# Optimization experiments

Hardware: AMD Instinct MI355X
Metric: run time of the kernel (lower is better)

Reference implementation:

```python
import jax, jax.numpy as jnp
import numpy as np
import math

EMBED = 768
HEADS = 12
DK = EMBED // HEADS
FFN = 3072
NQ = 8
B, S = 4, 2048


def _layernorm(x, g, b, eps=1e-5):
    mu = jnp.mean(x, axis=-1, keepdims=True)
    var = jnp.var(x, axis=-1, keepdims=True)
    return (x - mu) * jax.lax.rsqrt(var + eps) * g + b


def setup_inputs() -> dict:
    key = jax.random.key(0)
    ks = jax.random.split(key, 16)
    std = 0.02
    inp = {
        "x": jax.random.normal(ks[0], (B, S, EMBED), dtype=jnp.float32),
        "mask": jnp.ones((B, S), dtype=jnp.int32),
        # attention projections (torch Linear: W [out, in])
        "wq": jax.random.normal(ks[1], (EMBED, EMBED), jnp.float32) * std,
        "bq": jnp.zeros((EMBED,), jnp.float32),
        "wk": jax.random.normal(ks[2], (EMBED, EMBED), jnp.float32) * std,
        "bk": jnp.zeros((EMBED,), jnp.float32),
        "wv": jax.random.normal(ks[3], (EMBED, EMBED), jnp.float32) * std,
        "bv": jnp.zeros((EMBED,), jnp.float32),
        "wo": jax.random.normal(ks[4], (EMBED, EMBED), jnp.float32) * std,
        "bo": jnp.zeros((EMBED,), jnp.float32),
        # layernorms
        "g1": jnp.ones((EMBED,), jnp.float32),
        "be1": jnp.zeros((EMBED,), jnp.float32),
        "g2": jnp.ones((EMBED,), jnp.float32),
        "be2": jnp.zeros((EMBED,), jnp.float32),
        # quantum FFN: trainable RY angles + two linears
        "theta": jax.random.normal(ks[5], (NQ,), jnp.float32) * 0.1,
        "w1": jax.random.normal(ks[6], (FFN, NQ), jnp.float32) * std,
        "b1": jnp.zeros((FFN,), jnp.float32),
        "w2": jax.random.normal(ks[7], (EMBED, FFN), jnp.float32) * std,
        "b2": jnp.zeros((EMBED,), jnp.float32),
    }
    return inp


def _block(x, mask, wq, bq, wk, bk, wv, bv, wo, bo, g1, be1, g2, be2,
           theta, w1, b1, w2, b2):
    b, s, _ = x.shape
    # --- multi-head attention (dropout = identity at eval) ---
    q = (x @ wq.T + bq).reshape(b, s, HEADS, DK)
    k = (x @ wk.T + bk).reshape(b, s, HEADS, DK)
    v = (x @ wv.T + bv).reshape(b, s, HEADS, DK)
    scores = jnp.einsum("bqhd,bkhd->bhqk", q, k) / math.sqrt(DK)
    scores = jnp.where(mask[:, None, None, :] == 0, -1e9, scores)
    attn = jax.nn.softmax(scores, axis=-1)
    ctx = jnp.einsum("bhqk,bkhd->bqhd", attn, v).reshape(b, s, EMBED)
    attn_out = ctx @ wo.T + bo
    x = _layernorm(x + attn_out, g1, be1)
    # --- quantum FFN: RY(x_i) then RY(theta_i) on |0>, <Z> = cos(x_i+theta_i)
    # (product state, no entanglement -> exact closed form, fully batched)
    meas = jnp.cos(x[..., :NQ] + theta)            # [b, s, NQ]
    h = jax.nn.relu(meas @ w1.T + b1)              # [b, s, FFN]
    ffn_out = h @ w2.T + b2                        # [b, s, EMBED]
    return _layernorm(x + ffn_out, g2, be2)


def reference(x, mask, wq, bq, wk, bk, wv, bv, wo, bo, g1, be1, g2, be2,
              theta, w1, b1, w2, b2):
    return _block(x, mask, wq, bq, wk, bk, wv, bv, wo, bo,
                  g1, be1, g2, be2, theta, w1, b1, w2, b2)
```

## Files before the change

### kernel.cpp

```cpp
#include <hip/hip_runtime.h>
#include <hip/hip_bf16.h>


typedef __bf16 bf16_t;
typedef bf16_t bf16x4 __attribute__((ext_vector_type(4)));
typedef bf16_t bf16x8 __attribute__((ext_vector_type(8)));
typedef float floatx4 __attribute__((ext_vector_type(4)));

#define LOG2E 1.44269504088896f

__device__ __forceinline__ void gload16(const bf16_t* g, bf16_t* l) {
    __builtin_amdgcn_global_load_lds(
        (const __attribute__((address_space(1))) unsigned int*)g,
        (__attribute__((address_space(3))) unsigned int*)l,
        16, 0, 0);
}

__global__ __launch_bounds__(256)
void prep(const float* __restrict__ x,
          const float* __restrict__ wq, const float* __restrict__ wk,
          const float* __restrict__ wv, const float* __restrict__ wo,
          const float* __restrict__ w2, const float* __restrict__ w1,
          const float* __restrict__ bq, const float* __restrict__ bk,
          const float* __restrict__ bv, const int* __restrict__ mask,
          bf16_t* __restrict__ xb, bf16_t* __restrict__ wqkv,
          bf16_t* __restrict__ wob, bf16_t* __restrict__ w2b,
          bf16_t* __restrict__ w1b, float* __restrict__ bqkv,
          float* __restrict__ mbf)
{
    const int seg = blockIdx.y;
    const int idx = blockIdx.x * 256 + threadIdx.x;
    if (seg == 0) {
        if (idx >= 1572864) return;
        const float4 f = ((const float4*)x)[idx];
        bf16x4 o = {(bf16_t)f.x, (bf16_t)f.y, (bf16_t)f.z, (bf16_t)f.w};
        ((bf16x4*)xb)[idx] = o;
    } else if (seg == 1) {
        if (idx >= 442368) return;
        const int e = idx * 4;
        float4 f = (e < 589824) ? ((const float4*)wq)[idx]
                 : (e < 1179648) ? ((const float4*)wk)[idx - 147456]
                                 : ((const float4*)wv)[idx - 294912];
        if (e < 589824) { f.x *= 0.125f; f.y *= 0.125f; f.z *= 0.125f; f.w *= 0.125f; }
        bf16x4 o = {(bf16_t)f.x, (bf16_t)f.y, (bf16_t)f.z, (bf16_t)f.w};
        ((bf16x4*)wqkv)[idx] = o;
    } else if (seg == 2) {
        if (idx >= 147456) return;
        const float4 f = ((const float4*)wo)[idx];
        bf16x4 o = {(bf16_t)f.x, (bf16_t)f.y, (bf16_t)f.z, (bf16_t)f.w};
        ((bf16x4*)wob)[idx] = o;
    } else if (seg == 3) {
        if (idx >= 589824) return;
        const float4 f = ((const float4*)w2)[idx];
        bf16x4 o = {(bf16_t)f.x, (bf16_t)f.y, (bf16_t)f.z, (bf16_t)f.w};
        ((bf16x4*)w2b)[idx] = o;
    } else if (seg == 4) {
        if (idx >= 576) return;
        const int e = idx * 4;
        float4 f = (e < 768) ? ((const float4*)bq)[idx]
                 : (e < 1536) ? ((const float4*)bk)[idx - 192]
                              : ((const float4*)bv)[idx - 384];
        if (e < 768) { f.x *= 0.125f; f.y *= 0.125f; f.z *= 0.125f; f.w *= 0.125f; }
        ((float4*)bqkv)[idx] = f;
    } else if (seg == 5) {
        if (idx >= 6144) return;
        const float4 f = ((const float4*)w1)[idx];
        bf16x4 o = {(bf16_t)f.x, (bf16_t)f.y, (bf16_t)f.z, (bf16_t)f.w};
        ((bf16x4*)w1b)[idx] = o;
    } else {
        if (idx >= 2048) return;
        const int4 m = ((const int4*)mask)[idx];
        float4 f;
        f.x = (m.x == 0) ? -1e9f : 0.f;
        f.y = (m.y == 0) ? -1e9f : 0.f;
        f.z = (m.z == 0) ? -1e9f : 0.f;
        f.w = (m.w == 0) ? -1e9f : 0.f;
        ((float4*)mbf)[idx] = f;
    }
}

template<typename TC>
__global__ __launch_bounds__(256)
void gemm_bb(const bf16_t* __restrict__ A, const bf16_t* __restrict__ W,
             const float* __restrict__ bias, TC* __restrict__ C,
             int kPer, int lda, int ldw, int ldc, int splitStride)
{
    __shared__ __align__(16) bf16_t As[2][4096];
    __shared__ __align__(16) bf16_t Bs[2][4096];
    const int tid  = threadIdx.x;
    const int wave = tid >> 6;
    const int lane = tid & 63;
    const int wm = (wave >> 1) * 64;
    const int wn = (wave & 1) * 64;

    const int nwg  = gridDim.x * gridDim.y;
    const int flat = blockIdx.y * gridDim.x + blockIdx.x;
    const int swzb = (flat & 7) * (nwg >> 3) + (flat >> 3);
    const int bm = (swzb / gridDim.x) * 128;
    const int bn = (swzb % gridDim.x) * 128;

    const int fr = lane & 15;
    const int fk = (lane >> 4) * 8;

    const int kBeg = blockIdx.z * kPer;
    const int kEnd = kBeg + kPer;
    C += (size_t)blockIdx.z * splitStride;

    const int srow = tid >> 2;
    const int scol = (tid & 3) * 8;

    floatx4 acc[4][4] = {};

    const bf16_t* gA = A + (size_t)(bm + srow) * lda + scol;
    const bf16_t* gB = W + (size_t)(bn + srow) * ldw + scol;

#define STAGE(buf, kk)                                              \
    {   const bf16_t* ga = gA + (kk);                               \
        const bf16_t* gb = gB + (kk);                               \
        gload16(ga,                    &As[buf][tid * 8]);          \
        gload16(ga + (size_t)64 * lda, &As[buf][tid * 8 + 2048]);   \
        gload16(gb,                    &Bs[buf][tid * 8]);          \
        gload16(gb + (size_t)64 * ldw, &Bs[buf][tid * 8 + 2048]);   \
    }

    STAGE(0, kBeg);
    __syncthreads();

    int cur = 0;
    for (int k0 = kBeg; k0 < kEnd; k0 += 32) {
        if (k0 + 32 < kEnd) STAGE(cur ^ 1, k0 + 32);

        bf16x8 fa[4], fb[4];
        #pragma unroll
        for (int i = 0; i < 4; ++i) {
            fa[i] = *(const bf16x8*)&As[cur][(wm + i * 16 + fr) * 32 + fk];
            fb[i] = *(const bf16x8*)&Bs[cur][(wn + i * 16 + fr) * 32 + fk];
        }
        #pragma unroll
        for (int mi = 0; mi < 4; ++mi)
            #pragma unroll
            for (int ni = 0; ni < 4; ++ni)
                acc[mi][ni] = __builtin_amdgcn_mfma_f32_16x16x32_bf16(
                    fa[mi], fb[ni], acc[mi][ni], 0, 0, 0);

        __syncthreads();
        cur ^= 1;
    }
#undef STAGE

    const int fg = (lane >> 4) * 4;
    const bool addb = (blockIdx.z == 0);
    #pragma unroll
    for (int mi = 0; mi < 4; ++mi) {
        #pragma unroll
        for (int ni = 0; ni < 4; ++ni) {
            const int col = bn + wn + ni * 16 + fr;
            const float bv = addb ? bias[col] : 0.f;
            #pragma unroll
            for (int r = 0; r < 4; ++r) {
                const int row = bm + wm + mi * 16 + fg + r;
                C[(size_t)row * ldc + col] = (TC)(acc[mi][ni][r] + bv);
            }
        }
    }
}

__global__ __launch_bounds__(256)
void gemm_qkv(const bf16_t* __restrict__ A, const bf16_t* __restrict__ W0,
              const float* __restrict__ bias0,
              bf16_t* __restrict__ Qb, bf16_t* __restrict__ Kh,
              bf16_t* __restrict__ VhT)
{
    __shared__ __align__(16) bf16_t As[2][4096];
    __shared__ __align__(16) bf16_t Bs[2][4096];
    const int tid  = threadIdx.x;
    const int wave = tid >> 6;
    const int lane = tid & 63;
    const int wm = (wave >> 1) * 64;
    const int wn = (wave & 1) * 64;

    const int nwg  = gridDim.x * gridDim.y;
    const int flat = blockIdx.y * gridDim.x + blockIdx.x;
    const int swzb = (flat & 7) * (nwg >> 3) + (flat >> 3);
    const int tx = swzb % gridDim.x;
    const int bm = (swzb / gridDim.x) * 128;
    const int sect = tx / 6;
    const int bn = (tx % 6) * 128;
    const bf16_t* W    = W0 + (size_t)sect * 589824;
    const float* bias  = bias0 + sect * 768;

    const int fr = lane & 15;
    const int fk = (lane >> 4) * 8;
    const int srow = tid >> 2;
    const int scol = (tid & 3) * 8;

    floatx4 acc[4][4] = {};

    const bf16_t* gA = A + (size_t)(bm + srow) * 768 + scol;
    const bf16_t* gB = W + (size_t)(bn + srow) * 768 + scol;

#define STAGEQ(buf, kk)                                             \
    {   const bf16_t* ga = gA + (kk);                               \
        const bf16_t* gb = gB + (kk);                               \
        gload16(ga,                   &As[buf][tid * 8]);           \
        gload16(ga + (size_t)64*768,  &As[buf][tid * 8 + 2048]);    \
        gload16(gb,                   &Bs[buf][tid * 8]);           \
        gload16(gb + (size_t)64*768,  &Bs[buf][tid * 8 + 2048]);    \
    }

    STAGEQ(0, 0);
    __syncthreads();

    int cur = 0;
    for (int k0 = 0; k0 < 768; k0 += 32) {
        if (k0 + 32 < 768) STAGEQ(cur ^ 1, k0 + 32);

        bf16x8 fa[4], fb[4];
        #pragma unroll
        for (int i = 0; i < 4; ++i) {
            fa[i] = *(const bf16x8*)&As[cur][(wm + i * 16 + fr) * 32 + fk];
            fb[i] = *(const bf16x8*)&Bs[cur][(wn + i * 16 + fr) * 32 + fk];
        }
        #pragma unroll
        for (int mi = 0; mi < 4; ++mi)
            #pragma unroll
            for (int ni = 0; ni < 4; ++ni)
                acc[mi][ni] = __builtin_amdgcn_mfma_f32_16x16x32_bf16(
                    fa[mi], fb[ni], acc[mi][ni], 0, 0, 0);

        __syncthreads();
        cur ^= 1;
    }
#undef STAGEQ

    const int fg = (lane >> 4) * 4;
    #pragma unroll
    for (int mi = 0; mi < 4; ++mi) {
        const int row0 = bm + wm + mi * 16 + fg;
        #pragma unroll
        for (int ni = 0; ni < 4; ++ni) {
            const int col = bn + wn + ni * 16 + fr;
            const float bv = bias[col];
            if (sect == 0) {
                #pragma unroll
                for (int r = 0; r < 4; ++r)
                    Qb[(size_t)(row0 + r) * 768 + col] =
                        (bf16_t)(acc[mi][ni][r] + bv);
            } else if (sect == 1) {
                const int head = col >> 6;
                const int d    = col & 63;
                #pragma unroll
                for (int r = 0; r < 4; ++r) {
                    const int row = row0 + r;
                    const size_t base =
                        ((size_t)((row >> 11) * 12 + head) * 2048 + (row & 2047)) * 64;
                    Kh[base + (d ^ ((row & 7) << 3))] =
                        (bf16_t)(acc[mi][ni][r] + bv);
                }
            } else {
                const int head = col >> 6;
                const int d    = col & 63;
                bf16x4 v4;
                #pragma unroll
                for (int r = 0; r < 4; ++r)
                    v4[r] = (bf16_t)(acc[mi][ni][r] + bv);
                const int bhh = (row0 >> 11) * 12 + head;
                const int t   = row0 & 2047;
                const size_t idx = ((size_t)bhh * 64 + d) * 2048 +
                                   (t & ~63) + ((t & 63) ^ ((d & 7) << 3));
                *(bf16x4*)&VhT[idx] = v4;
            }
        }
    }
}

__global__ __launch_bounds__(256)
void attn_mfma(const bf16_t* __restrict__ Qb, const bf16_t* __restrict__ Kh,
               const bf16_t* __restrict__ VhT, const float* __restrict__ mbf,
               bf16_t* __restrict__ ctx)
{
    __shared__ __align__(16) bf16_t Ks[2][4096];
    __shared__ __align__(16) bf16_t Vt[2][4096];
    __shared__ bf16_t Vones[16 * 72];
    __shared__ bf16_t Pl[4][32][72];

    const int flat = blockIdx.x;
    const int swzb = (flat & 7) * 96 + (flat >> 3);
    const int bh = swzb >> 4;
    const int b = bh / 12, h = bh % 12;
    const int tid  = threadIdx.x;
    const int wave = tid >> 6;
    const int lane = tid & 63;
    const int g    = lane >> 4;
    const int fr   = lane & 15;
    const int qbase = (swzb & 15) * 128 + wave * 32;

    for (int idx = tid; idx < 16 * 72; idx += 256)
        Vones[idx] = (bf16_t)((idx < 72) ? 1.f : 0.f);

    bf16x8 qf[2][2];
    #pragma unroll
    for (int qt = 0; qt < 2; ++qt)
        #pragma unroll
        for (int s = 0; s < 2; ++s) {
            const size_t tok = (size_t)(b * 2048 + qbase + qt * 16 + fr);
            qf[qt][s] = *(const bf16x8*)(Qb + tok * 768 + h * 64 + s * 32 + g * 8);
        }

    floatx4 o[2][4] = {};
    floatx4 oe[2] = {};

    const bf16_t* kbase = Kh  + (size_t)bh * 131072;
    const bf16_t* vbase = VhT + (size_t)bh * 131072;
    const float*  mrow  = mbf + b * 2048;
    const size_t  voff  = (size_t)(tid >> 3) * 2048 + (tid & 7) * 8;

    gload16(kbase + tid * 8,        &Ks[0][tid * 8]);
    gload16(kbase + tid * 8 + 2048, &Ks[0][tid * 8 + 2048]);
    gload16(vbase + voff,             &Vt[0][tid * 8]);
    gload16(vbase + voff + 32 * 2048, &Vt[0][tid * 8 + 2048]);

    int cur = 0;
    for (int kt = 0; kt < 32; ++kt) {
        __syncthreads();

        if (kt + 1 < 32) {
            const bf16_t* kn = kbase + (kt + 1) * 4096;
            gload16(kn + tid * 8,        &Ks[cur ^ 1][tid * 8]);
            gload16(kn + tid * 8 + 2048, &Ks[cur ^ 1][tid * 8 + 2048]);
            const bf16_t* vn = vbase + (kt + 1) * 64;
            gload16(vn + voff,             &Vt[cur ^ 1][tid * 8]);
            gload16(vn + voff + 32 * 2048, &Vt[cur ^ 1][tid * 8 + 2048]);
        }

        floatx4 st_[2][4] = {};
        #pragma unroll
        for (int s = 0; s < 2; ++s) {
            bf16x8 kf[4];
            #pragma unroll
            for (int ct = 0; ct < 4; ++ct) {
                const int krow = ct * 16 + fr;
                const int kcol = (s * 32 + g * 8) ^ ((krow & 7) << 3);
                kf[ct] = *(const bf16x8*)&Ks[cur][krow * 64 + kcol];
            }
            #pragma unroll
            for (int qt = 0; qt < 2; ++qt)
                #pragma unroll
                for (int ct = 0; ct < 4; ++ct)
                    st_[qt][ct] = __builtin_amdgcn_mfma_f32_16x16x32_bf16(
                        kf[ct], qf[qt][s], st_[qt][ct], 0, 0, 0);
        }

        #pragma unroll
        for (int qt = 0; qt < 2; ++qt) {
            #pragma unroll
            for (int ct = 0; ct < 4; ++ct) {
                const float4 mb4 = *(const float4*)&mrow[kt * 64 + ct * 16 + g * 4];
                const float mbr[4] = { mb4.x, mb4.y, mb4.z, mb4.w };
                bf16x4 pw;
                #pragma unroll
                for (int r = 0; r < 4; ++r)
                    pw[r] = (bf16_t)__builtin_amdgcn_exp2f(
                        fmaf(st_[qt][ct][r], LOG2E, mbr[r]));
                *(bf16x4*)&Pl[wave][qt * 16 + fr][ct * 16 + g * 4] = pw;
            }
        }

        #pragma unroll
        for (int st2 = 0; st2 < 2; ++st2) {
            bf16x8 pf[2];
            #pragma unroll
            for (int qt = 0; qt < 2; ++qt)
                pf[qt] = *(const bf16x8*)&Pl[wave][qt * 16 + fr][st2 * 32 + g * 8];
            #pragma unroll
            for (int dt = 0; dt < 4; ++dt) {
                const int vrow = dt * 16 + fr;
                const int vcol = (st2 * 32 + g * 8) ^ ((vrow & 7) << 3);
                const bf16x8 vf = *(const bf16x8*)&Vt[cur][vrow * 64 + vcol];
                #pragma unroll
                for (int qt = 0; qt < 2; ++qt)
                    o[qt][dt] = __builtin_amdgcn_mfma_f32_16x16x32_bf16(
                        pf[qt], vf, o[qt][dt], 0, 0, 0);
            }
            const bf16x8 vo = *(const bf16x8*)&Vones[fr * 72 + st2 * 32 + g * 8];
            #pragma unroll
            for (int qt = 0; qt < 2; ++qt)
                oe[qt] = __builtin_amdgcn_mfma_f32_16x16x32_bf16(
                    pf[qt], vo, oe[qt], 0, 0, 0);
        }

        cur ^= 1;
    }

    #pragma unroll
    for (int qt = 0; qt < 2; ++qt) {
        float inv[4];
        #pragma unroll
        for (int r = 0; r < 4; ++r) {
            const float lv = __shfl(oe[qt][r], (lane & 48), 64);
            inv[r] = 1.f / lv;
        }
        #pragma unroll
        for (int dt = 0; dt < 4; ++dt)
            #pragma unroll
            for (int r = 0; r < 4; ++r) {
                const size_t row = (size_t)(b * 2048 + qbase + qt * 16 + g * 4 + r);
                ctx[row * 768 + h * 64 + dt * 16 + fr] = (bf16_t)(o[qt][dt][r] * inv[r]);
            }
    }
}

__global__ __launch_bounds__(256)
void ln_fuse(const float* __restrict__ xin, const float* __restrict__ proj,
             const float* __restrict__ proj2,
             const float* __restrict__ g, const float* __restrict__ be,
             float* __restrict__ out,
             const float* __restrict__ theta, float* __restrict__ meas)
{
    const int wave = threadIdx.x >> 6;
    const int lane = threadIdx.x & 63;
    const int row  = blockIdx.x * 4 + wave;
    const size_t base = (size_t)row * 768;

    float4 v[3];
    float s1 = 0.f, s2 = 0.f;
    #pragma unroll
    for (int i = 0; i < 3; ++i) {
        const int c4 = lane + i * 64;
        const float4 a  = ((const float4*)(xin  + base))[c4];
        const float4 p  = ((const float4*)(proj + base))[c4];
        const float4 p2 = ((const float4*)(proj2 + base))[c4];
        v[i].x = a.x + p.x + p2.x;
        v[i].y = a.y + p.y + p2.y;
        v[i].z = a.z + p.z + p2.z;
        v[i].w = a.w + p.w + p2.w;
        s1 += v[i].x + v[i].y + v[i].z + v[i].w;
        s2 += v[i].x*v[i].x + v[i].y*v[i].y + v[i].z*v[i].z + v[i].w*v[i].w;
    }
    #pragma unroll
    for (int mk = 32; mk >= 1; mk >>= 1) {
        s1 += __shfl_xor(s1, mk, 64);
        s2 += __shfl_xor(s2, mk, 64);
    }
    const float mu   = s1 * (1.f / 768.f);
    const float var  = s2 * (1.f / 768.f) - mu * mu;
    const float rinv = rsqrtf(var + 1e-5f);

    #pragma unroll
    for (int i = 0; i < 3; ++i) {
        const int c4 = lane + i * 64;
        const float4 gg = ((const float4*)g)[c4];
        const float4 bb = ((const float4*)be)[c4];
        float4 o;
        o.x = (v[i].x - mu) * rinv * gg.x + bb.x;
        o.y = (v[i].y - mu) * rinv * gg.y + bb.y;
        o.z = (v[i].z - mu) * rinv * gg.z + bb.z;
        o.w = (v[i].w - mu) * rinv * gg.w + bb.w;
        ((float4*)(out + base))[c4] = o;
        if (i == 0 && meas != nullptr && lane < 2) {
            meas[row * 8 + lane * 4 + 0] = cosf(o.x + theta[lane * 4 + 0]);
            meas[row * 8 + lane * 4 + 1] = cosf(o.y + theta[lane * 4 + 1]);
            meas[row * 8 + lane * 4 + 2] = cosf(o.z + theta[lane * 4 + 2]);
            meas[row * 8 + lane * 4 + 3] = cosf(o.w + theta[lane * 4 + 3]);
        }
    }
}

__global__ __launch_bounds__(256)
void ffn1(const float* __restrict__ meas, const bf16_t* __restrict__ w1b,
          const float* __restrict__ b1, bf16_t* __restrict__ h)
{
    const int row0 = blockIdx.x * 4;
    __shared__ float ms[4][8];
    if (threadIdx.x < 32)
        ms[threadIdx.x >> 3][threadIdx.x & 7] = meas[row0 * 8 + threadIdx.x];
    __syncthreads();
    #pragma unroll
    for (int i = 0; i < 12; ++i) {
        const int f = threadIdx.x + i * 256;
        const bf16x8 w = *(const bf16x8*)(w1b + f * 8);
        float wv[8];
        #pragma unroll
        for (int j = 0; j < 8; ++j) wv[j] = (float)w[j];
        const float bias = b1[f];
        #pragma unroll
        for (int r = 0; r < 4; ++r) {
            float v = bias;
            #pragma unroll
            for (int j = 0; j < 8; ++j) v += ms[r][j] * wv[j];
            h[(size_t)(row0 + r) * 3072 + f] = (bf16_t)fmaxf(v, 0.f);
        }
    }
}

extern "C" void kernel_launch(void* const* d_in, const int* in_sizes, int n_in,
                              void* d_out, int out_size, void* d_ws, size_t ws_size,
                              hipStream_t stream)
{
    const float* x     = (const float*)d_in[0];
    const int*   mask  = (const int*)d_in[1];
    const float* wq    = (const float*)d_in[2];
    const float* bq    = (const float*)d_in[3];
    const float* wk    = (const float*)d_in[4];
    const float* bk    = (const float*)d_in[5];
    const float* wv    = (const float*)d_in[6];
    const float* bv    = (const float*)d_in[7];
    const float* wo    = (const float*)d_in[8];
    const float* bo    = (const float*)d_in[9];
    const float* g1    = (const float*)d_in[10];
    const float* be1   = (const float*)d_in[11];
    const float* g2    = (const float*)d_in[12];
    const float* be2   = (const float*)d_in[13];
    const float* theta = (const float*)d_in[14];
    const float* w1    = (const float*)d_in[15];
    const float* b1    = (const float*)d_in[16];
    const float* w2    = (const float*)d_in[17];
    const float* b2    = (const float*)d_in[18];
    float* out = (float*)d_out;

    char* ws = (char*)d_ws;
    bf16_t* Qb     = (bf16_t*)(ws + 0);
    bf16_t* Kh     = (bf16_t*)(ws + 12582912);
    bf16_t* VhT    = (bf16_t*)(ws + 25165824);
    bf16_t* ctx    = (bf16_t*)(ws + 37748736);
    float*  attnp  = (float*)(ws + 50331648);
    float*  y      = (float*)(ws + 100663296);
    float*  meas   = (float*)(ws + 125829120);
    bf16_t* xb     = (bf16_t*)(ws + 126091264);
    bf16_t* wqkv   = (bf16_t*)(ws + 138674176);
    bf16_t* wob    = (bf16_t*)(ws + 142213120);
    bf16_t* w2b    = (bf16_t*)(ws + 143392768);
    float*  bqkv   = (float*)(ws + 148111360);
    bf16_t* w1b    = (bf16_t*)(ws + 148120576);
    float*  mbf    = (float*)(ws + 148169728);
    float*  ffnp   = (float*)(ws + 0);
    bf16_t* h      = (bf16_t*)(ws + 50331648);

    const dim3 blk(256);

    prep<<<dim3(6144, 7), blk, 0, stream>>>(x, wq, wk, wv, wo, w2, w1, bq, bk, bv,
                                            mask, xb, wqkv, wob, w2b, w1b, bqkv, mbf);

    gemm_qkv<<<dim3(18, 64), blk, 0, stream>>>(xb, wqkv, bqkv, Qb, Kh, VhT);

    attn_mfma<<<dim3(768), blk, 0, stream>>>(Qb, Kh, VhT, mbf, ctx);

    gemm_bb<float><<<dim3(6, 64, 2), blk, 0, stream>>>(
        ctx, wob, bo, attnp, 384, 768, 768, 768, 6291456);

    ln_fuse<<<dim3(2048), blk, 0, stream>>>(x, attnp, attnp + 6291456,
                                            g1, be1, y, theta, meas);

    ffn1<<<dim3(2048), blk, 0, stream>>>(meas, w1b, b1, h);

    gemm_bb<float><<<dim3(6, 64, 2), blk, 0, stream>>>(
        h, w2b, b2, ffnp, 1536, 3072, 3072, 768, 6291456);

    ln_fuse<<<dim3(2048), blk, 0, stream>>>(y, ffnp, ffnp + 6291456,
                                            g2, be2, out, nullptr, nullptr);
}
```

Measured before the change: 282.6 us.

## Store split-K GEMM partials in bf16 and fuse FFN1 into first layernorm

The two split-K GEMM outputs (attention out-projection and FFN2) now write bf16 partials instead of fp32. This halves the write and read traffic between each GEMM and its layernorm. The ffn1 kernel is folded into the first ln_fuse: the cos measurements stay in shared memory and the block computes the 3072-wide relu layer for its four rows, which removes one launch and the meas buffer round trip. It costs precision on the summed partials, and the fused layernorm kernel does much more work per block.

```diff
diff --git a/kernel.cpp b/kernel.cpp
--- a/kernel.cpp
+++ b/kernel.cpp
@@ -411,29 +411,31 @@
 }
 
 __global__ __launch_bounds__(256)
-void ln_fuse(const float* __restrict__ xin, const float* __restrict__ proj,
-             const float* __restrict__ proj2,
+void ln_fuse(const float* __restrict__ xin, const bf16_t* __restrict__ proj,
+             const bf16_t* __restrict__ proj2,
              const float* __restrict__ g, const float* __restrict__ be,
-             float* __restrict__ out,
-             const float* __restrict__ theta, float* __restrict__ meas)
+             float* __restrict__ out, const float* __restrict__ theta,
+             const bf16_t* __restrict__ w1b, const float* __restrict__ b1,
+             bf16_t* __restrict__ h)
 {
     const int wave = threadIdx.x >> 6;
     const int lane = threadIdx.x & 63;
     const int row  = blockIdx.x * 4 + wave;
     const size_t base = (size_t)row * 768;
+    __shared__ float ms[4][8];
 
     float4 v[3];
     float s1 = 0.f, s2 = 0.f;
     #pragma unroll
     for (int i = 0; i < 3; ++i) {
         const int c4 = lane + i * 64;
-        const float4 a  = ((const float4*)(xin  + base))[c4];
-        const float4 p  = ((const float4*)(proj + base))[c4];
-        const float4 p2 = ((const float4*)(proj2 + base))[c4];
-        v[i].x = a.x + p.x + p2.x;
-        v[i].y = a.y + p.y + p2.y;
-        v[i].z = a.z + p.z + p2.z;
-        v[i].w = a.w + p.w + p2.w;
+        const float4 a  = ((const float4*)(xin + base))[c4];
+        const bf16x4 p  = ((const bf16x4*)(proj + base))[c4];
+        const bf16x4 p2 = ((const bf16x4*)(proj2 + base))[c4];
+        v[i].x = a.x + (float)p[0] + (float)p2[0];
+        v[i].y = a.y + (float)p[1] + (float)p2[1];
+        v[i].z = a.z + (float)p[2] + (float)p2[2];
+        v[i].w = a.w + (float)p[3] + (float)p2[3];
         s1 += v[i].x + v[i].y + v[i].z + v[i].w;
         s2 += v[i].x*v[i].x + v[i].y*v[i].y + v[i].z*v[i].z + v[i].w*v[i].w;
     }
@@ -457,38 +459,32 @@
         o.z = (v[i].z - mu) * rinv * gg.z + bb.z;
         o.w = (v[i].w - mu) * rinv * gg.w + bb.w;
         ((float4*)(out + base))[c4] = o;
-        if (i == 0 && meas != nullptr && lane < 2) {
-            meas[row * 8 + lane * 4 + 0] = cosf(o.x + theta[lane * 4 + 0]);
-            meas[row * 8 + lane * 4 + 1] = cosf(o.y + theta[lane * 4 + 1]);
-            meas[row * 8 + lane * 4 + 2] = cosf(o.z + theta[lane * 4 + 2]);
-            meas[row * 8 + lane * 4 + 3] = cosf(o.w + theta[lane * 4 + 3]);
-        }
-    }
-}
-
-__global__ __launch_bounds__(256)
-void ffn1(const float* __restrict__ meas, const bf16_t* __restrict__ w1b,
-          const float* __restrict__ b1, bf16_t* __restrict__ h)
-{
-    const int row0 = blockIdx.x * 4;
-    __shared__ float ms[4][8];
-    if (threadIdx.x < 32)
-        ms[threadIdx.x >> 3][threadIdx.x & 7] = meas[row0 * 8 + threadIdx.x];
-    __syncthreads();
-    #pragma unroll
-    for (int i = 0; i < 12; ++i) {
-        const int f = threadIdx.x + i * 256;
-        const bf16x8 w = *(const bf16x8*)(w1b + f * 8);
-        float wv[8];
-        #pragma unroll
-        for (int j = 0; j < 8; ++j) wv[j] = (float)w[j];
-        const float bias = b1[f];
-        #pragma unroll
-        for (int r = 0; r < 4; ++r) {
-            float v = bias;
-            #pragma unroll
-            for (int j = 0; j < 8; ++j) v += ms[r][j] * wv[j];
-            h[(size_t)(row0 + r) * 3072 + f] = (bf16_t)fmaxf(v, 0.f);
+        if (i == 0 && w1b != nullptr && lane < 2) {
+            ms[wave][lane * 4 + 0] = cosf(o.x + theta[lane * 4 + 0]);
+            ms[wave][lane * 4 + 1] = cosf(o.y + theta[lane * 4 + 1]);
+            ms[wave][lane * 4 + 2] = cosf(o.z + theta[lane * 4 + 2]);
+            ms[wave][lane * 4 + 3] = cosf(o.w + theta[lane * 4 + 3]);
+        }
+    }
+
+    if (w1b != nullptr) {
+        __syncthreads();
+        const int row0 = blockIdx.x * 4;
+        #pragma unroll
+        for (int i = 0; i < 12; ++i) {
+            const int f = threadIdx.x + i * 256;
+            const bf16x8 w = *(const bf16x8*)(w1b + f * 8);
+            float wv[8];
+            #pragma unroll
+            for (int j = 0; j < 8; ++j) wv[j] = (float)w[j];
+            const float bias = b1[f];
+            #pragma unroll
+            for (int r = 0; r < 4; ++r) {
+                float vv = bias;
+                #pragma unroll
+                for (int j = 0; j < 8; ++j) vv += ms[r][j] * wv[j];
+                h[(size_t)(row0 + r) * 3072 + f] = (bf16_t)fmaxf(vv, 0.f);
+            }
         }
     }
 }
@@ -523,18 +519,17 @@
     bf16_t* Kh     = (bf16_t*)(ws + 12582912);
     bf16_t* VhT    = (bf16_t*)(ws + 25165824);
     bf16_t* ctx    = (bf16_t*)(ws + 37748736);
-    float*  attnp  = (float*)(ws + 50331648);
-    float*  y      = (float*)(ws + 100663296);
-    float*  meas   = (float*)(ws + 125829120);
-    bf16_t* xb     = (bf16_t*)(ws + 126091264);
-    bf16_t* wqkv   = (bf16_t*)(ws + 138674176);
-    bf16_t* wob    = (bf16_t*)(ws + 142213120);
-    bf16_t* w2b    = (bf16_t*)(ws + 143392768);
-    float*  bqkv   = (float*)(ws + 148111360);
-    bf16_t* w1b    = (bf16_t*)(ws + 148120576);
-    float*  mbf    = (float*)(ws + 148169728);
-    float*  ffnp   = (float*)(ws + 0);
-    bf16_t* h      = (bf16_t*)(ws + 50331648);
+    bf16_t* attnp  = (bf16_t*)(ws + 50331648);
+    bf16_t* h      = (bf16_t*)(ws + 0);
+    bf16_t* ffnp   = (bf16_t*)(ws + 50331648);
+    float*  y      = (float*)(ws + 75497472);
+    bf16_t* xb     = (bf16_t*)(ws + 100663296);
+    bf16_t* wqkv   = (bf16_t*)(ws + 113246208);
+    bf16_t* wob    = (bf16_t*)(ws + 116785152);
+    bf16_t* w2b    = (bf16_t*)(ws + 117964800);
+    float*  bqkv   = (float*)(ws + 122683392);
+    bf16_t* w1b    = (bf16_t*)(ws + 122692608);
+    float*  mbf    = (float*)(ws + 122741760);
 
     const dim3 blk(256);
 
@@ -545,17 +540,15 @@
 
     attn_mfma<<<dim3(768), blk, 0, stream>>>(Qb, Kh, VhT, mbf, ctx);
 
-    gemm_bb<float><<<dim3(6, 64, 2), blk, 0, stream>>>(
+    gemm_bb<bf16_t><<<dim3(6, 64, 2), blk, 0, stream>>>(
         ctx, wob, bo, attnp, 384, 768, 768, 768, 6291456);
 
     ln_fuse<<<dim3(2048), blk, 0, stream>>>(x, attnp, attnp + 6291456,
-                                            g1, be1, y, theta, meas);
-
-    ffn1<<<dim3(2048), blk, 0, stream>>>(meas, w1b, b1, h);
-
-    gemm_bb<float><<<dim3(6, 64, 2), blk, 0, stream>>>(
+                                            g1, be1, y, theta, w1b, b1, h);
+
+    gemm_bb<bf16_t><<<dim3(6, 64, 2), blk, 0, stream>>>(
         h, w2b, b2, ffnp, 1536, 3072, 3072, 768, 6291456);
 
     ln_fuse<<<dim3(2048), blk, 0, stream>>>(y, ffnp, ffnp + 6291456,
-                                            g2, be2, out, nullptr, nullptr);
-}
+                                            g2, be2, out, theta, nullptr, nullptr, nullptr);
+}
```

After: 266.5 us (median of 3 runs). -5.7%, faster.
